# Kernel optimization log

Measured on AMD Instinct MI355X. Metric: run time of the kernel, lower is better.

Reference implementation:

```python
import jax, jax.numpy as jnp
import numpy as np
import math

V, B, C, H, W = 4, 8, 512, 16, 16
NH = 8


def setup_inputs() -> dict:
    key = jax.random.key(0)
    ks = jax.random.split(key, 10)
    def n(k, shape, s=1.0):
        return jax.random.normal(k, shape, dtype=jnp.float32) * s
    return dict(
        i=n(ks[0], (V, B, C, H, W)),
        c=n(ks[1], (V, B, C, H, W)),
        j=n(ks[2], (V, B, C, H, W)),
        ln1_g=jnp.ones((C,), jnp.float32), ln1_b=jnp.zeros((C,), jnp.float32),
        ln2_g=jnp.ones((C,), jnp.float32), ln2_b=jnp.zeros((C,), jnp.float32),
        Wq=n(ks[3], (C, C), 0.02), bq=jnp.zeros((C,), jnp.float32),
        Wkv=n(ks[4], (C, 2 * C), 0.02), bkv=jnp.zeros((2 * C,), jnp.float32),
        Wo=n(ks[5], (C, C), 0.02), bo=jnp.zeros((C,), jnp.float32),
        Wfc=n(ks[6], (C, 4 * C), 0.02), bfc=jnp.zeros((4 * C,), jnp.float32),
        Wpr=n(ks[7], (4 * C, C), 0.02), bpr=jnp.zeros((C,), jnp.float32),
    )


def _ln(x, g, b, eps=1e-5):
    mu = jnp.mean(x, axis=-1, keepdims=True)
    var = jnp.mean((x - mu) ** 2, axis=-1, keepdims=True)
    return (x - mu) * jax.lax.rsqrt(var + eps) * g + b


def _gelu_new(x):
    # 0.5*x*(1+tanh(sqrt(2/pi)*(x+0.044715*x^3)))
    k = math.sqrt(2.0 / math.pi)
    return 0.5 * x * (1.0 + jnp.tanh(k * (x + 0.044715 * x ** 3)))


def reference(i, c, j, ln1_g, ln1_b, ln2_g, ln2_b, Wq, bq, Wkv, bkv, Wo, bo, Wfc, bfc, Wpr, bpr):
    v, b, ch, h, w = i.shape
    T = v * h * w
    hd = ch // NH

    def to_seq(x):  # v b c h w -> b (v h w) c
        return jnp.transpose(x, (1, 0, 3, 4, 2)).reshape(b, T, ch)

    # LayerNorm (over channel dim) applied before attention
    qs = _ln(to_seq(i), ln1_g, ln1_b)   # [b, T, c]
    kvs = _ln(to_seq(j), ln1_g, ln1_b)  # [b, T, c]

    q = qs @ Wq + bq                    # [b, T, c]
    kv = kvs @ Wkv + bkv                # [b, T, 2c]
    k, vv = jnp.split(kv, 2, axis=-1)

    def heads(x):  # [b, T, c] -> [b, nh, T, hd]
        return x.reshape(b, T, NH, hd).transpose(0, 2, 1, 3)
    q, k, vv = heads(q), heads(k), heads(vv)

    # block-causal mask: token in view-block r attends to view-blocks <= r
    blk = jnp.arange(T) // (h * w)
    mask = blk[:, None] >= blk[None, :]  # [T, T] bool

    att = jnp.einsum('bhqd,bhkd->bhqk', q, k) * (1.0 / math.sqrt(hd))
    att = jnp.where(mask, att, -jnp.inf)
    att = jax.nn.softmax(att, axis=-1)
    y = jnp.einsum('bhqk,bhkd->bhqd', att, vv)
    y = y.transpose(0, 2, 1, 3).reshape(b, T, ch)
    y = y @ Wo + bo                     # attention output, seq layout

    # residual: ln1(c) + attn
    cs = _ln(to_seq(c), ln1_g, ln1_b) + y
    # MLP with residual
    hcs = _ln(cs, ln2_g, ln2_b)
    cs = cs + (_gelu_new(hcs @ Wfc + bfc) @ Wpr + bpr)

    # b (v h w) c -> v b c h w
    out = cs.reshape(b, v, h, w, ch).transpose(1, 0, 4, 2, 3)
    return out
```

## Files before the change

### kernel.cpp

```cpp
#include <hip/hip_runtime.h>
#include <hip/hip_bf16.h>
#include <math.h>


typedef __bf16 bf16;
typedef __bf16 bf16x8 __attribute__((ext_vector_type(8)));
typedef __bf16 bf16x4 __attribute__((ext_vector_type(4)));
typedef float  f32x4  __attribute__((ext_vector_type(4)));

__device__ __forceinline__ void gload_lds16(const void* g, void* l) {
  __builtin_amdgcn_global_load_lds(
      (__attribute__((address_space(1))) void*)(g),
      (__attribute__((address_space(3))) void*)(l), 16, 0, 0);
}

__global__ __launch_bounds__(256)
void prep_k(const float* __restrict__ Wq, const float* __restrict__ Wkv,
            const float* __restrict__ Wo, const float* __restrict__ Wfc,
            const float* __restrict__ Wpr,
            bf16* __restrict__ WqT, bf16* __restrict__ WkvT,
            bf16* __restrict__ WoT, bf16* __restrict__ WfcT,
            bf16* __restrict__ WprT,
            const float* __restrict__ xi, const float* __restrict__ xj,
            const float* __restrict__ xc,
            const float* __restrict__ g, const float* __restrict__ bb,
            bf16* __restrict__ qs, bf16* __restrict__ kvs,
            bf16* __restrict__ csb)
{
  __shared__ float tile[64 * 65];
  __shared__ float red[4][64];
  const int t = blockIdx.x;
  const int tid = threadIdx.x;
  if (t < 768) {
    const float* W; bf16* Wt; int K, N, nx, tl;
    if (t < 64)        { W = Wq;  Wt = WqT;  K = 512;  N = 512;  nx = 8;  tl = t; }
    else if (t < 192)  { W = Wkv; Wt = WkvT; K = 512;  N = 1024; nx = 16; tl = t - 64; }
    else if (t < 256)  { W = Wo;  Wt = WoT;  K = 512;  N = 512;  nx = 8;  tl = t - 192; }
    else if (t < 512)  { W = Wfc; Wt = WfcT; K = 512;  N = 2048; nx = 32; tl = t - 256; }
    else               { W = Wpr; Wt = WprT; K = 2048; N = 512;  nx = 8;  tl = t - 512; }
    const int bx = tl % nx, by = tl / nx;
    const int n0 = bx << 6, k0 = by << 6;
    const int xl = tid & 15, yl = tid >> 4;
#pragma unroll
    for (int r = 0; r < 4; ++r) {
      const int row = yl + r * 16;
      const f32x4 vv = *(const f32x4*)&W[(size_t)(k0 + row) * N + n0 + xl * 4];
#pragma unroll
      for (int e = 0; e < 4; ++e)
        tile[row * 65 + xl * 4 + e] = vv[e];
    }
    __syncthreads();
    const int xk = tid & 7, nl = tid >> 3;
#pragma unroll
    for (int r2 = 0; r2 < 2; ++r2) {
      const int n = nl + r2 * 32;
      bf16x8 o;
#pragma unroll
      for (int e = 0; e < 8; ++e)
        o[e] = (bf16)tile[(xk * 8 + e) * 65 + n];
      *(bf16x8*)&Wt[(size_t)(n0 + n) * K + k0 + xk * 8] = o;
    }
    return;
  }
  const int u = t - 768;
  const int sel = u >> 8, bid = u & 255;
  const int hp = bid & 7, b = (bid >> 3) & 7, v = bid >> 6;
  const float* src = (sel == 0) ? xi : ((sel == 1) ? xj : xc);
  const size_t base = ((size_t)(v * 8 + b) * 512) * 256 + hp * 32;
  const int q8 = tid & 7, chb = tid >> 3;
  const int wid = tid >> 6, lc = (tid >> 3) & 7;
  const int cb = chb << 4;

  float gr[16], br[16];
#pragma unroll
  for (int p = 0; p < 4; ++p) {
    *(f32x4*)&gr[p * 4] = *(const f32x4*)&g[cb + p * 4];
    *(f32x4*)&br[p * 4] = *(const f32x4*)&bb[cb + p * 4];
  }
  f32x4 x[16];
#pragma unroll
  for (int k = 0; k < 16; ++k)
    x[k] = *(const f32x4*)&src[base + (size_t)(cb + k) * 256 + q8 * 4];

  float s[4] = {0.f, 0.f, 0.f, 0.f}, ss[4] = {0.f, 0.f, 0.f, 0.f};
#pragma unroll
  for (int k = 0; k < 16; ++k)
#pragma unroll
    for (int i = 0; i < 4; ++i) {
      s[i] += x[k][i];
      ss[i] += x[k][i] * x[k][i];
    }
#pragma unroll
  for (int off = 8; off < 64; off <<= 1)
#pragma unroll
    for (int i = 0; i < 4; ++i) {
      s[i] += __shfl_xor(s[i], off);
      ss[i] += __shfl_xor(ss[i], off);
    }
  if (lc < 4)      red[wid][q8 * 4 + lc]            = s[lc];
  else             red[wid][32 + q8 * 4 + (lc - 4)] = ss[lc - 4];
  __syncthreads();
  f32x4 st = {0.f, 0.f, 0.f, 0.f}, sst = {0.f, 0.f, 0.f, 0.f};
#pragma unroll
  for (int w = 0; w < 4; ++w) {
    st  += *(const f32x4*)&red[w][q8 * 4];
    sst += *(const f32x4*)&red[w][32 + q8 * 4];
  }
  float mu[4], rs[4];
#pragma unroll
  for (int i = 0; i < 4; ++i) {
    mu[i] = st[i] * (1.f / 512.f);
    rs[i] = rsqrtf(sst[i] * (1.f / 512.f) - mu[i] * mu[i] + 1e-5f);
  }
  bf16* dstb = (sel == 0) ? qs : ((sel == 1) ? kvs : csb);
  const int tkb = v * 256 + hp * 32 + q8 * 4;
#pragma unroll
  for (int i = 0; i < 4; ++i) {
    const size_t orow = ((size_t)b * 1024 + tkb + i) * 512 + cb;
    bf16x8 o0, o1;
#pragma unroll
    for (int k = 0; k < 8; ++k) {
      o0[k] = (bf16)((x[k][i] - mu[i]) * rs[i] * gr[k] + br[k]);
      o1[k] = (bf16)((x[k + 8][i] - mu[i]) * rs[i] * gr[k + 8] + br[k + 8]);
    }
    *(bf16x8*)&dstb[orow]     = o0;
    *(bf16x8*)&dstb[orow + 8] = o1;
  }
}

__global__ __launch_bounds__(256)
void ln2_k(const bf16* __restrict__ cs, const float* __restrict__ g,
           const float* __restrict__ bb, bf16* __restrict__ hcs)
{
  const int tid = threadIdx.x, wid = tid >> 6, lane = tid & 63;
  const int row = blockIdx.x * 4 + wid;
  const bf16x8 v8 = *(const bf16x8*)&cs[(size_t)row * 512 + lane * 8];
  float v[8];
#pragma unroll
  for (int k = 0; k < 8; ++k) v[k] = (float)v8[k];
  float s = 0.f, ss = 0.f;
#pragma unroll
  for (int k = 0; k < 8; ++k) { s += v[k]; ss += v[k] * v[k]; }
#pragma unroll
  for (int off = 1; off < 64; off <<= 1) {
    s += __shfl_xor(s, off);
    ss += __shfl_xor(ss, off);
  }
  const float mu = s * (1.f / 512.f);
  const float rstd = rsqrtf(ss * (1.f / 512.f) - mu * mu + 1e-5f);
  bf16x8 o;
#pragma unroll
  for (int k = 0; k < 8; ++k) {
    int ch = lane * 8 + k;
    o[k] = (bf16)((v[k] - mu) * rstd * g[ch] + bb[ch]);
  }
  *(bf16x8*)&hcs[(size_t)row * 512 + lane * 8] = o;
}

__global__ __launch_bounds__(256)
void gemm_fc_k(const bf16* __restrict__ A, const bf16* __restrict__ Bt,
               const float* __restrict__ bias, bf16* __restrict__ fo)
{
  const int K = 512;
  __shared__ __align__(16) char smem[34816];
  bf16* As = (bf16*)smem;
  bf16* Bs = (bf16*)(smem + 16384);
  const int tid = threadIdx.x;
  const int wid = tid >> 6, lane = tid & 63;
  const int wr = wid >> 1, wc = wid & 1;
  const int ml = lane & 15, kg = (lane >> 4) << 3;
  const int m0 = blockIdx.x * 128, n0 = blockIdx.y * 128;

  const int e0 = wid * 512 + lane * 8;
  const int r0 = e0 >> 5, c0 = e0 & 31;
  const int e1 = e0 + 2048;
  const int r1 = e1 >> 5, c1 = e1 & 31;

  const bf16* Ag = A + (size_t)m0 * K;
  const bf16* Bg = Bt + (size_t)n0 * K;

  f32x4 acc[4][4] = {};

  gload_lds16(Ag + (size_t)r0 * K + c0, As + wid * 512);
  gload_lds16(Ag + (size_t)r1 * K + c1, As + 2048 + wid * 512);
  gload_lds16(Bg + (size_t)r0 * K + c0, Bs + wid * 512);
  gload_lds16(Bg + (size_t)r1 * K + c1, Bs + 2048 + wid * 512);

  int cur = 0;
  for (int k0 = 0; k0 < K; k0 += 32) {
    __syncthreads();
    if (k0 + 32 < K) {
      const int nb = cur ^ 1, kn = k0 + 32;
      gload_lds16(Ag + (size_t)r0 * K + kn + c0, As + nb * 4096 + wid * 512);
      gload_lds16(Ag + (size_t)r1 * K + kn + c1, As + nb * 4096 + 2048 + wid * 512);
      gload_lds16(Bg + (size_t)r0 * K + kn + c0, Bs + nb * 4096 + wid * 512);
      gload_lds16(Bg + (size_t)r1 * K + kn + c1, Bs + nb * 4096 + 2048 + wid * 512);
    }
    bf16x8 af[4], bfr[4];
#pragma unroll
    for (int mf = 0; mf < 4; ++mf)
      af[mf] = *(const bf16x8*)&As[cur * 4096 + (wr * 64 + mf * 16 + ml) * 32 + kg];
#pragma unroll
    for (int nf = 0; nf < 4; ++nf)
      bfr[nf] = *(const bf16x8*)&Bs[cur * 4096 + (wc * 64 + nf * 16 + ml) * 32 + kg];
#pragma unroll
    for (int mf = 0; mf < 4; ++mf)
#pragma unroll
      for (int nf = 0; nf < 4; ++nf)
        acc[mf][nf] = __builtin_amdgcn_mfma_f32_16x16x32_bf16(
            af[mf], bfr[nf], acc[mf][nf], 0, 0, 0);
    cur ^= 1;
  }

  __syncthreads();
  bf16* OT = (bf16*)smem;
  const int jrow0 = (lane >> 4) << 2;
#pragma unroll
  for (int nf = 0; nf < 4; ++nf) {
    const float bv = bias[n0 + wc * 64 + nf * 16 + ml];
#pragma unroll
    for (int mf = 0; mf < 4; ++mf)
#pragma unroll
      for (int j = 0; j < 4; ++j) {
        float x = acc[mf][nf][j] + bv;
        float u = 0.7978845608f * (x + 0.044715f * x * x * x);
        float e = __expf(2.f * u);
        float th = 1.f - 2.f / (e + 1.f);
        OT[(wr * 64 + mf * 16 + jrow0 + j) * 132 + wc * 64 + nf * 16 + ml] =
            (bf16)(0.5f * x * (1.f + th));
      }
  }
  __syncthreads();
#pragma unroll
  for (int it = 0; it < 8; ++it) {
    const int idx = it * 256 + tid;
    const int cg = idx & 15, r = idx >> 4;
    *(bf16x8*)&fo[(size_t)(m0 + r) * 2048 + n0 + cg * 8] =
        *(const bf16x8*)&OT[r * 132 + cg * 8];
  }
}

enum { EPI_O = 2, EPI_PR = 4 };

template <int EPI>
__global__ __launch_bounds__(512)
void gemmsk_k(const bf16* __restrict__ A, const bf16* __restrict__ Bt,
              const float* __restrict__ bias, const bf16* res,
              void* out0, int K)
{
  __shared__ __align__(16) char smem[49152];
  bf16*  AS = (bf16*)smem;
  bf16*  BS = (bf16*)(smem + 16384);
  float* CF = (float*)smem;

  const int tid = threadIdx.x;
  const int wid = tid >> 6, lane = tid & 63;
  const int half = wid >> 2, w2 = wid & 3;
  const int wr = w2 >> 1, wc = w2 & 1;
  const int ml = lane & 15, kg = (lane >> 4) << 3;
  const int m0 = blockIdx.x * 64, n0 = blockIdx.y * 128;
  const int Kh = K >> 1;

  const int eA = w2 * 512 + lane * 8;
  const int rA = eA >> 5, cA = eA & 31;
  const int eB0 = (w2 * 2) * 512 + lane * 8;
  const int rB0 = eB0 >> 5, cB0 = eB0 & 31;
  const int eB1 = eB0 + 512;
  const int rB1 = eB1 >> 5, cB1 = eB1 & 31;

  const bf16* Ag = A + (size_t)m0 * K + half * Kh;
  const bf16* Bg = Bt + (size_t)n0 * K + half * Kh;

  f32x4 acc[2][4] = {};

  gload_lds16(Ag + (size_t)rA * K + cA, AS + half * 2048 + w2 * 512);
  gload_lds16(Bg + (size_t)rB0 * K + cB0, BS + half * 4096 + (w2 * 2) * 512);
  gload_lds16(Bg + (size_t)rB1 * K + cB1, BS + half * 4096 + (w2 * 2 + 1) * 512);

  int cur = 0;
  for (int k0 = 0; k0 < Kh; k0 += 32) {
    __syncthreads();
    if (k0 + 32 < Kh) {
      const int kn = k0 + 32, nb = cur ^ 1;
      gload_lds16(Ag + (size_t)rA * K + kn + cA,
                  AS + nb * 4096 + half * 2048 + w2 * 512);
      gload_lds16(Bg + (size_t)rB0 * K + kn + cB0,
                  BS + nb * 8192 + half * 4096 + (w2 * 2) * 512);
      gload_lds16(Bg + (size_t)rB1 * K + kn + cB1,
                  BS + nb * 8192 + half * 4096 + (w2 * 2 + 1) * 512);
    }
    const bf16* Ac = AS + cur * 4096 + half * 2048;
    const bf16* Bc = BS + cur * 8192 + half * 4096;
    bf16x8 af[2], bfr[4];
#pragma unroll
    for (int mf = 0; mf < 2; ++mf)
      af[mf] = *(const bf16x8*)&Ac[(wr * 32 + mf * 16 + ml) * 32 + kg];
#pragma unroll
    for (int nf = 0; nf < 4; ++nf)
      bfr[nf] = *(const bf16x8*)&Bc[(wc * 64 + nf * 16 + ml) * 32 + kg];
#pragma unroll
    for (int mf = 0; mf < 2; ++mf)
#pragma unroll
      for (int nf = 0; nf < 4; ++nf)
        acc[mf][nf] = __builtin_amdgcn_mfma_f32_16x16x32_bf16(
            af[mf], bfr[nf], acc[mf][nf], 0, 0, 0);
    cur ^= 1;
  }

  const int jrow0 = (lane >> 4) << 2;
  __syncthreads();
  if (half == 0) {
#pragma unroll
    for (int mf = 0; mf < 2; ++mf)
#pragma unroll
      for (int nf = 0; nf < 4; ++nf)
#pragma unroll
        for (int j = 0; j < 4; ++j)
          CF[(wr * 32 + mf * 16 + jrow0 + j) * 128 + wc * 64 + nf * 16 + ml] =
              acc[mf][nf][j];
  }
  __syncthreads();
  if (half == 1) {
#pragma unroll
    for (int nf = 0; nf < 4; ++nf) {
      const int n = n0 + wc * 64 + nf * 16 + ml;
      const float bv = bias[n];
#pragma unroll
      for (int mf = 0; mf < 2; ++mf) {
        const int mbase = m0 + wr * 32 + mf * 16 + jrow0;
        float v4[4];
#pragma unroll
        for (int j = 0; j < 4; ++j)
          v4[j] = acc[mf][nf][j] +
                  CF[(wr * 32 + mf * 16 + jrow0 + j) * 128 + wc * 64 + nf * 16 + ml];
        if constexpr (EPI == EPI_O) {
          bf16* cs = (bf16*)out0;
#pragma unroll
          for (int j = 0; j < 4; ++j) {
            const size_t idx = (size_t)(mbase + j) * 512 + n;
            cs[idx] = (bf16)(v4[j] + bv + (float)res[idx]);
          }
        } else {
          float* out = (float*)out0;
          const int b = mbase >> 10, t = mbase & 1023;
          const int v = t >> 8, hhh = (t >> 4) & 15, w0 = t & 15;
          f32x4 o;
#pragma unroll
          for (int j = 0; j < 4; ++j)
            o[j] = v4[j] + bv + (float)res[(size_t)(mbase + j) * 512 + n];
          *(f32x4*)&out[(((size_t)v * 8 + b) * 512 + n) * 256 + hhh * 16 + w0] = o;
        }
      }
    }
  }
}

__global__ __launch_bounds__(256)
void gemm_qkv_k(const bf16* __restrict__ Aq, const bf16* __restrict__ Akv,
                const bf16* __restrict__ WqT, const bf16* __restrict__ WkvT,
                const float* __restrict__ bq, const float* __restrict__ bkv,
                bf16* __restrict__ q_buf, bf16* __restrict__ k_buf,
                bf16* __restrict__ v_t)
{
  const int K = 512;
  __shared__ __align__(16) char smem[34816];
  bf16* As = (bf16*)smem;
  bf16* Bs = (bf16*)(smem + 16384);
  const int tid = threadIdx.x;
  const int wid = tid >> 6, lane = tid & 63;
  const int wr = wid >> 1, wc = wid & 1;
  const int ml = lane & 15, kg = (lane >> 4) << 3;
  const int ybl = blockIdx.y;
  const bool isq = ybl < 4;
  const bf16* A     = isq ? Aq  : Akv;
  const bf16* Bt    = isq ? WqT : WkvT;
  const float* bias = isq ? bq : bkv;
  const int n0 = isq ? (ybl << 7) : ((ybl - 4) << 7);
  const int m0 = blockIdx.x * 128;

  const int e0 = wid * 512 + lane * 8;
  const int r0 = e0 >> 5, c0 = e0 & 31;
  const int e1 = e0 + 2048;
  const int r1 = e1 >> 5, c1 = e1 & 31;

  const bf16* Ag = A + (size_t)m0 * K;
  const bf16* Bg = Bt + (size_t)n0 * K;

  f32x4 acc[4][4] = {};

  gload_lds16(Ag + (size_t)r0 * K + c0, As + wid * 512);
  gload_lds16(Ag + (size_t)r1 * K + c1, As + 2048 + wid * 512);
  gload_lds16(Bg + (size_t)r0 * K + c0, Bs + wid * 512);
  gload_lds16(Bg + (size_t)r1 * K + c1, Bs + 2048 + wid * 512);

  int cur = 0;
  for (int k0 = 0; k0 < K; k0 += 32) {
    __syncthreads();
    if (k0 + 32 < K) {
      const int nb = cur ^ 1, kn = k0 + 32;
      gload_lds16(Ag + (size_t)r0 * K + kn + c0, As + nb * 4096 + wid * 512);
      gload_lds16(Ag + (size_t)r1 * K + kn + c1, As + nb * 4096 + 2048 + wid * 512);
      gload_lds16(Bg + (size_t)r0 * K + kn + c0, Bs + nb * 4096 + wid * 512);
      gload_lds16(Bg + (size_t)r1 * K + kn + c1, Bs + nb * 4096 + 2048 + wid * 512);
    }
    bf16x8 af[4], bfr[4];
#pragma unroll
    for (int mf = 0; mf < 4; ++mf)
      af[mf] = *(const bf16x8*)&As[cur * 4096 + (wr * 64 + mf * 16 + ml) * 32 + kg];
#pragma unroll
    for (int nf = 0; nf < 4; ++nf)
      bfr[nf] = *(const bf16x8*)&Bs[cur * 4096 + (wc * 64 + nf * 16 + ml) * 32 + kg];
#pragma unroll
    for (int mf = 0; mf < 4; ++mf)
#pragma unroll
      for (int nf = 0; nf < 4; ++nf)
        acc[mf][nf] = __builtin_amdgcn_mfma_f32_16x16x32_bf16(
            af[mf], bfr[nf], acc[mf][nf], 0, 0, 0);
    cur ^= 1;
  }

  __syncthreads();
  bf16* OT = (bf16*)smem;
  const int jrow0 = (lane >> 4) << 2;
  const int b = m0 >> 10, t0 = m0 & 1023;
  if (ybl < 8) {
#pragma unroll
    for (int nf = 0; nf < 4; ++nf) {
      const float bv = bias[n0 + wc * 64 + nf * 16 + ml];
#pragma unroll
      for (int mf = 0; mf < 4; ++mf)
#pragma unroll
        for (int j = 0; j < 4; ++j)
          OT[(wr * 64 + mf * 16 + jrow0 + j) * 132 + wc * 64 + nf * 16 + ml] =
              (bf16)(acc[mf][nf][j] + bv);
    }
    __syncthreads();
    bf16* dst = isq ? q_buf : k_buf;
    const int h0 = n0 >> 6;
#pragma unroll
    for (int it = 0; it < 8; ++it) {
      const int idx = it * 256 + tid;
      const int dg = idx & 7, r = (idx >> 3) & 127, hl = idx >> 10;
      *(bf16x8*)&dst[(((size_t)b * 8 + h0 + hl) * 1024 + t0 + r) * 64 + dg * 8] =
          *(const bf16x8*)&OT[r * 132 + hl * 64 + dg * 8];
    }
  } else {
#pragma unroll
    for (int nf = 0; nf < 4; ++nf) {
      const float bv = bias[n0 + wc * 64 + nf * 16 + ml];
#pragma unroll
      for (int mf = 0; mf < 4; ++mf) {
        bf16x4 o;
#pragma unroll
        for (int j = 0; j < 4; ++j) o[j] = (bf16)(acc[mf][nf][j] + bv);
        *(bf16x4*)&OT[(wc * 64 + nf * 16 + ml) * 132 + wr * 64 + mf * 16 + jrow0] = o;
      }
    }
    __syncthreads();
    const int h0 = (n0 - 512) >> 6;
#pragma unroll
    for (int it = 0; it < 8; ++it) {
      const int idx = it * 256 + tid;
      const int og = idx & 15, c = idx >> 4;
      const int hl = c >> 6, d = c & 63;
      *(bf16x8*)&v_t[(((size_t)b * 8 + h0 + hl) * 64 + d) * 1024 + t0 + og * 8] =
          *(const bf16x8*)&OT[c * 132 + og * 8];
    }
  }
}

__global__ __launch_bounds__(512)
void attn_k(const bf16* __restrict__ qb, const bf16* __restrict__ kb,
            const bf16* __restrict__ vt, bf16* __restrict__ y)
{
  __shared__ bf16 Ks[2][4096];
  __shared__ bf16 Vs[2][4096];
  __shared__ bf16 Ps[8][1024];
  const int tid = threadIdx.x, wid = tid >> 6, lane = tid & 63;
  const int L = blockIdx.x;
  const int xcd = L & 7, chunk = L >> 3;
  const int bh = xcd + ((chunk >> 3) << 3);
  const int qt = 7 - (chunk & 7);
  const int b = bh >> 3, h = bh & 7;
  const int t0 = qt << 7;
  const int ml = lane & 15, hi = lane >> 4, kg = hi << 3;

  const bf16* qrow = qb + ((size_t)bh * 1024 + t0 + wid * 16) * 64;
  bf16x8 aq[2];
  aq[0] = *(const bf16x8*)&qrow[ml * 64 + kg];
  aq[1] = *(const bf16x8*)&qrow[ml * 64 + 32 + kg];

  f32x4 accO[4] = {};
  float lsum[4] = {0.f, 0.f, 0.f, 0.f};

  const int nkt = ((qt >> 1) + 1) << 2;
  const bf16* kbase = kb + (size_t)bh * 1024 * 64;
  const bf16* vbase = vt + (size_t)bh * 64 * 1024;

  const int sr = tid >> 3;
  const int sg = ((tid & 7) ^ (sr & 7)) << 3;
  bf16* pw = &Ps[wid][0];

  gload_lds16(kbase + (size_t)sr * 64 + sg,   &Ks[0][wid * 512]);
  gload_lds16(vbase + (size_t)sr * 1024 + sg, &Vs[0][wid * 512]);

  int cur = 0;
  for (int kt = 0; kt < nkt; ++kt) {
    __syncthreads();
    if (kt + 1 < nkt) {
      const int tk0 = (kt + 1) << 6;
      const int nb = cur ^ 1;
      gload_lds16(kbase + (size_t)(tk0 + sr) * 64 + sg,   &Ks[nb][wid * 512]);
      gload_lds16(vbase + (size_t)sr * 1024 + tk0 + sg,   &Vs[nb][wid * 512]);
    }

    f32x4 sa[4] = {};
    __builtin_amdgcn_s_setprio(1);
#pragma unroll
    for (int nf = 0; nf < 4; ++nf) {
      const int row = nf * 16 + ml;
#pragma unroll
      for (int ks = 0; ks < 2; ++ks) {
        const int g = ((ks * 4 + hi) ^ (ml & 7)) << 3;
        bf16x8 bk = *(const bf16x8*)&Ks[cur][row * 64 + g];
        sa[nf] = __builtin_amdgcn_mfma_f32_16x16x32_bf16(aq[ks], bk, sa[nf], 0, 0, 0);
      }
    }
    __builtin_amdgcn_s_setprio(0);

#pragma unroll
    for (int nf = 0; nf < 4; ++nf) {
      const int gp0 = nf * 2 + (ml >> 3);
#pragma unroll
      for (int j = 0; j < 4; ++j) {
        const float p = __expf(sa[nf][j] * 0.125f);
        lsum[j] += p;
        const int prow = (hi << 2) + j;
        pw[prow * 64 + ((gp0 ^ (prow & 7)) << 3) + (ml & 7)] = (bf16)p;
      }
    }

    __builtin_amdgcn_s_setprio(1);
#pragma unroll
    for (int ks = 0; ks < 2; ++ks) {
      const int g = ((ks * 4 + hi) ^ (ml & 7)) << 3;
      bf16x8 pa = *(const bf16x8*)&pw[ml * 64 + g];
#pragma unroll
      for (int df = 0; df < 4; ++df) {
        bf16x8 bv = *(const bf16x8*)&Vs[cur][(df * 16 + ml) * 64 + g];
        accO[df] = __builtin_amdgcn_mfma_f32_16x16x32_bf16(pa, bv, accO[df], 0, 0, 0);
      }
    }
    __builtin_amdgcn_s_setprio(0);
    cur ^= 1;
  }

  float inv[4];
#pragma unroll
  for (int j = 0; j < 4; ++j) {
    float s = lsum[j];
#pragma unroll
    for (int off = 1; off < 16; off <<= 1) s += __shfl_xor(s, off);
    inv[j] = 1.f / s;
  }
#pragma unroll
  for (int df = 0; df < 4; ++df)
#pragma unroll
    for (int j = 0; j < 4; ++j) {
      const int t = t0 + wid * 16 + (hi << 2) + j;
      const int c = h * 64 + df * 16 + ml;
      y[((size_t)b * 1024 + t) * 512 + c] = (bf16)(accO[df][j] * inv[j]);
    }
}

extern "C" void kernel_launch(void* const* d_in, const int* in_sizes, int n_in,
                              void* d_out, int out_size, void* d_ws, size_t ws_size,
                              hipStream_t stream)
{
  const float* xi    = (const float*)d_in[0];
  const float* xc    = (const float*)d_in[1];
  const float* xj    = (const float*)d_in[2];
  const float* ln1_g = (const float*)d_in[3];
  const float* ln1_b = (const float*)d_in[4];
  const float* ln2_g = (const float*)d_in[5];
  const float* ln2_b = (const float*)d_in[6];
  const float* Wq    = (const float*)d_in[7];
  const float* bq    = (const float*)d_in[8];
  const float* Wkv   = (const float*)d_in[9];
  const float* bkv   = (const float*)d_in[10];
  const float* Wo    = (const float*)d_in[11];
  const float* bo    = (const float*)d_in[12];
  const float* Wfc   = (const float*)d_in[13];
  const float* bfc   = (const float*)d_in[14];
  const float* Wpr   = (const float*)d_in[15];
  const float* bpr   = (const float*)d_in[16];

  char* ws = (char*)d_ws;
  const size_t MB = 1ull << 20;
  bf16*  qs    = (bf16*)(ws + 0);
  bf16*  kvs   = (bf16*)(ws + 8 * MB);
  bf16*  csb   = (bf16*)(ws + 16 * MB);
  bf16*  WqT   = (bf16*)(ws + 32 * MB);
  bf16*  WkvT  = (bf16*)(ws + 32 * MB + 512 * 1024);
  bf16*  WoT   = (bf16*)(ws + 33 * MB + 512 * 1024);
  bf16*  WfcT  = (bf16*)(ws + 34 * MB);
  bf16*  WprT  = (bf16*)(ws + 36 * MB);
  bf16*  q_buf = (bf16*)(ws + 38 * MB);
  bf16*  k_buf = (bf16*)(ws + 46 * MB);
  bf16*  v_t   = (bf16*)(ws + 54 * MB);
  bf16*  yb    = (bf16*)(ws + 0);
  bf16*  hcs   = (bf16*)(ws + 8 * MB);
  bf16*  fcact = (bf16*)(ws + 38 * MB);

  prep_k<<<dim3(1536), 256, 0, stream>>>(Wq, Wkv, Wo, Wfc, Wpr,
                                         WqT, WkvT, WoT, WfcT, WprT,
                                         xi, xj, xc, ln1_g, ln1_b, qs, kvs, csb);

  gemm_qkv_k<<<dim3(64, 12), 256, 0, stream>>>(qs, kvs, WqT, WkvT, bq, bkv,
                                               q_buf, k_buf, v_t);

  attn_k<<<dim3(512), 512, 0, stream>>>(q_buf, k_buf, v_t, yb);

  gemmsk_k<EPI_O><<<dim3(128, 4), 512, 0, stream>>>(yb, WoT, bo, csb,
                                                    (void*)csb, 512);

  ln2_k<<<dim3(2048), 256, 0, stream>>>(csb, ln2_g, ln2_b, hcs);

  gemm_fc_k<<<dim3(64, 16), 256, 0, stream>>>(hcs, WfcT, bfc, fcact);

  gemmsk_k<EPI_PR><<<dim3(128, 4), 512, 0, stream>>>(fcact, WprT, bpr, csb,
                                                     d_out, 2048);

  (void)in_sizes; (void)n_in; (void)out_size; (void)ws_size;
}
```

Measured before the change: 155.2 us.

## Remap GEMM blocks per XCD and widen FC GEMM tile to 128x256

The four GEMM kernels now use a 1D grid. Block ids are remapped so that consecutive blocks on the same XCD (bid&7) share M row tiles, which is meant to improve L2 reuse of the A operand across N tiles. The FC GEMM also moves from a 128x128 tile with 256 threads to a 128x256 tile with 512 threads, so each A tile is reused across more output columns. The cost is LDS use roughly doubling to about 68KB per block, which lowers occupancy, and half as many blocks for the FC kernel.

```diff
diff --git a/kernel.cpp b/kernel.cpp
--- a/kernel.cpp
+++ b/kernel.cpp
@@ -157,44 +157,42 @@
   *(bf16x8*)&hcs[(size_t)row * 512 + lane * 8] = o;
 }
 
-__global__ __launch_bounds__(256)
+__global__ __launch_bounds__(512)
 void gemm_fc_k(const bf16* __restrict__ A, const bf16* __restrict__ Bt,
                const float* __restrict__ bias, bf16* __restrict__ fo)
 {
   const int K = 512;
-  __shared__ __align__(16) char smem[34816];
+  __shared__ __align__(16) char smem[69632];
   bf16* As = (bf16*)smem;
   bf16* Bs = (bf16*)(smem + 16384);
+  bf16* OT = (bf16*)smem;
   const int tid = threadIdx.x;
   const int wid = tid >> 6, lane = tid & 63;
-  const int wr = wid >> 1, wc = wid & 1;
+  const int wr = wid >> 2, wcc = wid & 3;
   const int ml = lane & 15, kg = (lane >> 4) << 3;
-  const int m0 = blockIdx.x * 128, n0 = blockIdx.y * 128;
-
-  const int e0 = wid * 512 + lane * 8;
-  const int r0 = e0 >> 5, c0 = e0 & 31;
-  const int e1 = e0 + 2048;
-  const int r1 = e1 >> 5, c1 = e1 & 31;
-
+  const int bid = blockIdx.x;
+  const int xcd = bid & 7, chunk = bid >> 3;
+  const int m0 = (xcd * 8 + (chunk & 7)) * 128;
+  const int n0 = (chunk >> 3) * 256;
+
+  const int rA = (wid << 4) + (lane >> 2), cA = (lane & 3) << 3;
   const bf16* Ag = A + (size_t)m0 * K;
   const bf16* Bg = Bt + (size_t)n0 * K;
 
   f32x4 acc[4][4] = {};
 
-  gload_lds16(Ag + (size_t)r0 * K + c0, As + wid * 512);
-  gload_lds16(Ag + (size_t)r1 * K + c1, As + 2048 + wid * 512);
-  gload_lds16(Bg + (size_t)r0 * K + c0, Bs + wid * 512);
-  gload_lds16(Bg + (size_t)r1 * K + c1, Bs + 2048 + wid * 512);
+  gload_lds16(Ag + (size_t)rA * K + cA,         As + wid * 512);
+  gload_lds16(Bg + (size_t)rA * K + cA,         Bs + wid * 512);
+  gload_lds16(Bg + (size_t)(rA + 128) * K + cA, Bs + 4096 + wid * 512);
 
   int cur = 0;
   for (int k0 = 0; k0 < K; k0 += 32) {
     __syncthreads();
     if (k0 + 32 < K) {
       const int nb = cur ^ 1, kn = k0 + 32;
-      gload_lds16(Ag + (size_t)r0 * K + kn + c0, As + nb * 4096 + wid * 512);
-      gload_lds16(Ag + (size_t)r1 * K + kn + c1, As + nb * 4096 + 2048 + wid * 512);
-      gload_lds16(Bg + (size_t)r0 * K + kn + c0, Bs + nb * 4096 + wid * 512);
-      gload_lds16(Bg + (size_t)r1 * K + kn + c1, Bs + nb * 4096 + 2048 + wid * 512);
+      gload_lds16(Ag + (size_t)rA * K + kn + cA,         As + nb * 4096 + wid * 512);
+      gload_lds16(Bg + (size_t)rA * K + kn + cA,         Bs + nb * 8192 + wid * 512);
+      gload_lds16(Bg + (size_t)(rA + 128) * K + kn + cA, Bs + nb * 8192 + 4096 + wid * 512);
     }
     bf16x8 af[4], bfr[4];
 #pragma unroll
@@ -202,7 +200,7 @@
       af[mf] = *(const bf16x8*)&As[cur * 4096 + (wr * 64 + mf * 16 + ml) * 32 + kg];
 #pragma unroll
     for (int nf = 0; nf < 4; ++nf)
-      bfr[nf] = *(const bf16x8*)&Bs[cur * 4096 + (wc * 64 + nf * 16 + ml) * 32 + kg];
+      bfr[nf] = *(const bf16x8*)&Bs[cur * 8192 + (wcc * 64 + nf * 16 + ml) * 32 + kg];
 #pragma unroll
     for (int mf = 0; mf < 4; ++mf)
 #pragma unroll
@@ -213,11 +211,10 @@
   }
 
   __syncthreads();
-  bf16* OT = (bf16*)smem;
   const int jrow0 = (lane >> 4) << 2;
 #pragma unroll
   for (int nf = 0; nf < 4; ++nf) {
-    const float bv = bias[n0 + wc * 64 + nf * 16 + ml];
+    const float bv = bias[n0 + wcc * 64 + nf * 16 + ml];
 #pragma unroll
     for (int mf = 0; mf < 4; ++mf)
 #pragma unroll
@@ -226,17 +223,17 @@
         float u = 0.7978845608f * (x + 0.044715f * x * x * x);
         float e = __expf(2.f * u);
         float th = 1.f - 2.f / (e + 1.f);
-        OT[(wr * 64 + mf * 16 + jrow0 + j) * 132 + wc * 64 + nf * 16 + ml] =
+        OT[(wr * 64 + mf * 16 + jrow0 + j) * 264 + wcc * 64 + nf * 16 + ml] =
             (bf16)(0.5f * x * (1.f + th));
       }
   }
   __syncthreads();
 #pragma unroll
   for (int it = 0; it < 8; ++it) {
-    const int idx = it * 256 + tid;
-    const int cg = idx & 15, r = idx >> 4;
+    const int idx = it * 512 + tid;
+    const int cg = idx & 31, r = idx >> 5;
     *(bf16x8*)&fo[(size_t)(m0 + r) * 2048 + n0 + cg * 8] =
-        *(const bf16x8*)&OT[r * 132 + cg * 8];
+        *(const bf16x8*)&OT[r * 264 + cg * 8];
   }
 }
 
@@ -258,7 +255,10 @@
   const int half = wid >> 2, w2 = wid & 3;
   const int wr = w2 >> 1, wc = w2 & 1;
   const int ml = lane & 15, kg = (lane >> 4) << 3;
-  const int m0 = blockIdx.x * 64, n0 = blockIdx.y * 128;
+  const int bid = blockIdx.x;
+  const int xcd = bid & 7, chunk = bid >> 3;
+  const int m0 = (xcd * 16 + (chunk & 15)) * 64;
+  const int n0 = (chunk >> 4) * 128;
   const int Kh = K >> 1;
 
   const int eA = w2 * 512 + lane * 8;
@@ -370,13 +370,15 @@
   const int wid = tid >> 6, lane = tid & 63;
   const int wr = wid >> 1, wc = wid & 1;
   const int ml = lane & 15, kg = (lane >> 4) << 3;
-  const int ybl = blockIdx.y;
+  const int bid = blockIdx.x;
+  const int xcd = bid & 7, chunk = bid >> 3;
+  const int m0 = (xcd * 8 + (chunk & 7)) * 128;
+  const int ybl = chunk >> 3;
   const bool isq = ybl < 4;
   const bf16* A     = isq ? Aq  : Akv;
   const bf16* Bt    = isq ? WqT : WkvT;
   const float* bias = isq ? bq : bkv;
   const int n0 = isq ? (ybl << 7) : ((ybl - 4) << 7);
-  const int m0 = blockIdx.x * 128;
 
   const int e0 = wid * 512 + lane * 8;
   const int r0 = e0 >> 5, c0 = e0 & 31;
@@ -616,20 +618,20 @@
                                          WqT, WkvT, WoT, WfcT, WprT,
                                          xi, xj, xc, ln1_g, ln1_b, qs, kvs, csb);
 
-  gemm_qkv_k<<<dim3(64, 12), 256, 0, stream>>>(qs, kvs, WqT, WkvT, bq, bkv,
-                                               q_buf, k_buf, v_t);
+  gemm_qkv_k<<<dim3(768), 256, 0, stream>>>(qs, kvs, WqT, WkvT, bq, bkv,
+                                            q_buf, k_buf, v_t);
 
   attn_k<<<dim3(512), 512, 0, stream>>>(q_buf, k_buf, v_t, yb);
 
-  gemmsk_k<EPI_O><<<dim3(128, 4), 512, 0, stream>>>(yb, WoT, bo, csb,
-                                                    (void*)csb, 512);
+  gemmsk_k<EPI_O><<<dim3(512), 512, 0, stream>>>(yb, WoT, bo, csb,
+                                                 (void*)csb, 512);
 
   ln2_k<<<dim3(2048), 256, 0, stream>>>(csb, ln2_g, ln2_b, hcs);
 
-  gemm_fc_k<<<dim3(64, 16), 256, 0, stream>>>(hcs, WfcT, bfc, fcact);
-
-  gemmsk_k<EPI_PR><<<dim3(128, 4), 512, 0, stream>>>(fcact, WprT, bpr, csb,
-                                                     d_out, 2048);
+  gemm_fc_k<<<dim3(512), 512, 0, stream>>>(hcs, WfcT, bfc, fcact);
+
+  gemmsk_k<EPI_PR><<<dim3(512), 512, 0, stream>>>(fcact, WprT, bpr, csb,
+                                                  d_out, 2048);
 
   (void)in_sizes; (void)n_in; (void)out_size; (void)ws_size;
 }
```

After: 153.1 us. About the same (-1.4%).
